# Kernel tuning notes

Measured on AMD Instinct MI355X. Metric: run time of the kernel, lower is better.

## Reference

```python
import jax, jax.numpy as jnp
import numpy as np

B, N = 1, 320  # embed_dim == seq_len == N is forced by the module's bmm shapes


def setup_inputs() -> dict:
    key = jax.random.key(0)
    k1, k2, k3, k4 = jax.random.split(key, 4)
    s = jax.random.normal(k1, (B, N, N), dtype=jnp.float32)
    futrue = jax.random.normal(k2, (B, N, N, N), dtype=jnp.float32)
    # nn.Linear(embed_dim, embed_dim) params
    lim = 1.0 / np.sqrt(N)
    W = jax.random.uniform(k3, (N, N), minval=-lim, maxval=lim, dtype=jnp.float32)
    b = jax.random.uniform(k4, (N,), minval=-lim, maxval=lim, dtype=jnp.float32)
    return {"s": s, "futrue": futrue, "W": W, "b": b}


def reference(s, futrue, W, b):
    # futrue = self.fc(futrue): Linear on last dim  [B,T,T,E]
    futP = jnp.einsum('bitj,ej->bite', futrue, W) + b
    # fc = s.transpose(1,2) @ futrue : [B,1,E,T] @ [B,T,T,E] -> [B,T,E,E]
    scores = jnp.einsum('bte,bitj->biej', s, futP)
    fc = jax.nn.softmax(scores, axis=-1)          # softmax over last dim
    # vectorized loop: t_i = fc[:, i].sum(1).unsqueeze(-2).bmm(s)
    w = fc.sum(axis=2)                            # [B, T, T] (sum over e)
    out = jnp.einsum('bij,bjk->bik', w, s)        # concat of all t_i -> [B, T, E]
    return out
```

## Files before the change

kernel.cpp:

```cpp
#include <hip/hip_runtime.h>
#include <hip/hip_bf16.h>
#include <math.h>

#define N 320
#define NN (N * N)
#define AST 328
#define SST 324

typedef float f32x16 __attribute__((ext_vector_type(16)));
typedef short s16x8  __attribute__((ext_vector_type(8)));

#define MFMA32(a, b, c) __builtin_amdgcn_mfma_f32_32x32x16_bf16((a), (b), (c), 0, 0, 0)

union U4V { uint4 q; s16x8 v; };
union UAV { unsigned u[4]; s16x8 v; };
union BFU { __hip_bfloat16 b; unsigned short u; };

__device__ inline void bsplit(float x, unsigned short& h, unsigned short& l) {
    __hip_bfloat16 hb = __float2bfloat16(x);
    float r = __bfloat162float(hb);
    __hip_bfloat16 lb = __float2bfloat16(x - r);
    BFU a; a.b = hb; h = a.u;
    BFU c; c.b = lb; l = c.u;
}
__device__ inline void split2(float x0, float x1, unsigned& hi, unsigned& lo) {
    unsigned short h0, l0, h1, l1;
    bsplit(x0, h0, l0); bsplit(x1, h1, l1);
    hi = (unsigned)h0 | ((unsigned)h1 << 16);
    lo = (unsigned)l0 | ((unsigned)l1 << 16);
}

__global__ __launch_bounds__(256) void zero_w_kernel(float* __restrict__ w) {
    int idx = blockIdx.x * 256 + threadIdx.x;
    ((float4*)w)[idx] = make_float4(0.f, 0.f, 0.f, 0.f);
}

__global__ __launch_bounds__(64) void colsum_kernel(const float* __restrict__ s,
                                                    float* __restrict__ colsum) {
    int e = blockIdx.x * 64 + threadIdx.x;
    float acc = 0.f;
    for (int t = 0; t < N; ++t) acc += s[t * N + e];
    colsum[e] = acc;
}

__global__ __launch_bounds__(64) void pack_s_kernel(const float* __restrict__ s,
                                                    uint4* __restrict__ spH,
                                                    uint4* __restrict__ spL) {
    int blk = blockIdx.x;
    int l = threadIdx.x;
    int et = blk / 20, ts = blk % 20;
    int e = et * 32 + (l & 31);
    int t0 = ts * 16 + (l >> 5) * 8;
    unsigned hi[4], lo[4];
#pragma unroll
    for (int d = 0; d < 4; ++d) {
        float x0 = s[(t0 + 2 * d) * N + e];
        float x1 = s[(t0 + 2 * d + 1) * N + e];
        split2(x0, x1, hi[d], lo[d]);
    }
    spH[blk * 64 + l] = make_uint4(hi[0], hi[1], hi[2], hi[3]);
    spL[blk * 64 + l] = make_uint4(lo[0], lo[1], lo[2], lo[3]);
}

__global__ __launch_bounds__(64) void pack_w_kernel(const float* __restrict__ W,
                                                    uint4* __restrict__ wpH,
                                                    uint4* __restrict__ wpL) {
    int blk = blockIdx.x;
    int l = threadIdx.x;
    int jt = blk / 20, ks = blk % 20;
    int j = jt * 32 + (l & 31);
    int k0 = ks * 16 + (l >> 5) * 8;
    const float* wr = W + (size_t)j * N + k0;
    unsigned hi[4], lo[4];
#pragma unroll
    for (int d = 0; d < 4; ++d) split2(wr[2 * d], wr[2 * d + 1], hi[d], lo[d]);
    wpH[blk * 64 + l] = make_uint4(hi[0], hi[1], hi[2], hi[3]);
    wpL[blk * 64 + l] = make_uint4(lo[0], lo[1], lo[2], lo[3]);
}

__global__ __launch_bounds__(640, 5) void fused_kernel(
    const float* __restrict__ fut,
    const uint4* __restrict__ spH, const uint4* __restrict__ spL,
    const uint4* __restrict__ wpH, const uint4* __restrict__ wpL,
    const float* __restrict__ bvec, const float* __restrict__ colsum,
    float* __restrict__ w)
{
    const int i   = blockIdx.y;
    const int et  = blockIdx.x;
    const int tid = threadIdx.x;
    const int wid = tid >> 6;
    const int lane = tid & 63;
    const int l31 = lane & 31;
    const int hf  = lane >> 5;

    __shared__ union {
        struct { unsigned short H[32 * AST]; unsigned short L[32 * AST]; } a;
        float S[32 * SST];
    } sm;
    __shared__ float csh[32];
    __shared__ float Mfin[32];
    __shared__ float Ifin[32];

    if (tid < 32) csh[tid] = colsum[et * 32 + tid];

    f32x16 acc;
#pragma unroll
    for (int r = 0; r < 16; ++r) acc[r] = 0.f;

    const float* fbase = fut + (size_t)i * NN + (size_t)(hf * 8) * N + wid * 32 + l31;
    const uint4* aH = spH + (size_t)(et * 20) * 64 + lane;
    const uint4* aL = spL + (size_t)(et * 20) * 64 + lane;

    for (int ts = 0; ts < 20; ++ts) {
        const float* fp = fbase + (size_t)(ts * 16) * N;
        float f[8];
#pragma unroll
        for (int j = 0; j < 8; ++j) f[j] = fp[j * N];
        U4V ah; ah.q = aH[ts * 64];
        U4V al; al.q = aL[ts * 64];
        UAV bh, bl;
#pragma unroll
        for (int d = 0; d < 4; ++d) split2(f[2 * d], f[2 * d + 1], bh.u[d], bl.u[d]);
        acc = MFMA32(ah.v, bh.v, acc);
        acc = MFMA32(al.v, bh.v, acc);
        acc = MFMA32(ah.v, bl.v, acc);
    }

#pragma unroll
    for (int r = 0; r < 16; ++r) {
        int e = (r & 3) + ((r >> 2) << 3) + (hf << 2);
        unsigned short h, l;
        bsplit(acc[r], h, l);
        sm.a.H[e * AST + wid * 32 + l31] = h;
        sm.a.L[e * AST + wid * 32 + l31] = l;
    }
    __syncthreads();

    f32x16 acc2;
#pragma unroll
    for (int r = 0; r < 16; ++r) acc2[r] = 0.f;

    const uint4* bH = wpH + (size_t)(wid * 20) * 64 + lane;
    const uint4* bL = wpL + (size_t)(wid * 20) * 64 + lane;

    for (int ks = 0; ks < 20; ++ks) {
        int aoff = l31 * AST + ks * 16 + hf * 8;
        s16x8 gah = *(const s16x8*)&sm.a.H[aoff];
        s16x8 gal = *(const s16x8*)&sm.a.L[aoff];
        U4V wh; wh.q = bH[ks * 64];
        U4V wl; wl.q = bL[ks * 64];
        acc2 = MFMA32(gah, wh.v, acc2);
        acc2 = MFMA32(gal, wh.v, acc2);
        acc2 = MFMA32(gah, wl.v, acc2);
    }

    const int jcol = wid * 32 + l31;
    float bj = bvec[jcol];
    float v[16];
#pragma unroll
    for (int r = 0; r < 16; ++r) {
        int e = (r & 3) + ((r >> 2) << 3) + (hf << 2);
        v[r] = acc2[r] + csh[e] * bj;
    }

    __syncthreads();

#pragma unroll
    for (int r = 0; r < 16; ++r) {
        int e = (r & 3) + ((r >> 2) << 3) + (hf << 2);
        sm.S[e * SST + jcol] = v[r];
    }
    __syncthreads();

    const int hw = tid >> 5;
    const int li = tid & 31;
    if (hw < 16) {
#pragma unroll
        for (int rr = 0; rr < 2; ++rr) {
            int row = 2 * hw + rr;
            float x[10];
            float m = -3.4e38f;
#pragma unroll
            for (int q = 0; q < 10; ++q) {
                x[q] = sm.S[row * SST + li + 32 * q];
                m = fmaxf(m, x[q]);
            }
#pragma unroll
            for (int off = 16; off; off >>= 1) m = fmaxf(m, __shfl_xor(m, off, 64));
            float ssum = 0.f;
#pragma unroll
            for (int q = 0; q < 10; ++q) ssum += __expf(x[q] - m);
#pragma unroll
            for (int off = 16; off; off >>= 1) ssum += __shfl_xor(ssum, off, 64);
            if (li == 0) { Mfin[row] = m; Ifin[row] = 1.0f / ssum; }
        }
    }
    __syncthreads();

    float wcol = 0.f;
#pragma unroll
    for (int r = 0; r < 16; ++r) {
        int e = (r & 3) + ((r >> 2) << 3) + (hf << 2);
        wcol += __expf(v[r] - Mfin[e]) * Ifin[e];
    }
    wcol += __shfl_xor(wcol, 32, 64);
    if (hf == 0) atomicAdd(&w[(size_t)i * N + jcol], wcol);
}

__global__ __launch_bounds__(64) void out_gemm_kernel(
    const float* __restrict__ w, const float* __restrict__ s,
    float* __restrict__ out)
{
    const int k = blockIdx.x * 64 + threadIdx.x;
    const int i = blockIdx.y;
    const float* wr = w + (size_t)i * N;
    float acc = 0.f;
    for (int j = 0; j < N; ++j) acc += wr[j] * s[j * N + k];
    out[(size_t)i * N + k] = acc;
}

extern "C" void kernel_launch(void* const* d_in, const int* in_sizes, int n_in,
                              void* d_out, int out_size, void* d_ws, size_t ws_size,
                              hipStream_t stream)
{
    const float* s    = (const float*)d_in[0];
    const float* fut  = (const float*)d_in[1];
    const float* W    = (const float*)d_in[2];
    const float* bvec = (const float*)d_in[3];
    float* out = (float*)d_out;

    char* base = (char*)d_ws;
    float* wbuf   = (float*)base;
    float* colsum = (float*)(base + 409600);
    uint4* spH = (uint4*)(base + 410880);
    uint4* spL = (uint4*)(base + 615680);
    uint4* wpH = (uint4*)(base + 820480);
    uint4* wpL = (uint4*)(base + 1025280);

    zero_w_kernel<<<dim3(NN / 4 / 256), dim3(256), 0, stream>>>(wbuf);
    colsum_kernel<<<dim3(N / 64), dim3(64), 0, stream>>>(s, colsum);
    pack_s_kernel<<<dim3(200), dim3(64), 0, stream>>>(s, spH, spL);
    pack_w_kernel<<<dim3(200), dim3(64), 0, stream>>>(W, wpH, wpL);

    fused_kernel<<<dim3(10, N), dim3(640), 0, stream>>>(
        fut, spH, spL, wpH, wpL, bvec, colsum, wbuf);

    out_gemm_kernel<<<dim3(N / 64, N), dim3(64), 0, stream>>>(wbuf, s, out);
}
```

Before: 451.6 us.

## Swizzle LDS staging, remap block order, cheapen bf16 split, parallelize small kernels

The fused kernel's intermediate now goes through a chunked, XOR-swizzled LDS layout instead of a padded row layout, to cut bank conflicts on the second GEMM's operand reads. The grid becomes 1D and is remapped so groups of 8 consecutive i values share an et tile. The bf16 hi/lo split now uses bit truncation instead of round-to-nearest conversions, which is fewer instructions but changes the rounding of the hi part. Colsum is split across row chunks and combined with atomics, and out_gemm uses wider blocks with four partial accumulators.

```diff
diff --git a/kernel.cpp b/kernel.cpp
--- a/kernel.cpp
+++ b/kernel.cpp
@@ -4,8 +4,8 @@
 
 #define N 320
 #define NN (N * N)
-#define AST 328
 #define SST 324
+#define ZCNT (NN + N)
 
 typedef float f32x16 __attribute__((ext_vector_type(16)));
 typedef short s16x8  __attribute__((ext_vector_type(8)));
@@ -14,33 +14,33 @@
 
 union U4V { uint4 q; s16x8 v; };
 union UAV { unsigned u[4]; s16x8 v; };
-union BFU { __hip_bfloat16 b; unsigned short u; };
-
-__device__ inline void bsplit(float x, unsigned short& h, unsigned short& l) {
-    __hip_bfloat16 hb = __float2bfloat16(x);
-    float r = __bfloat162float(hb);
-    __hip_bfloat16 lb = __float2bfloat16(x - r);
-    BFU a; a.b = hb; h = a.u;
-    BFU c; c.b = lb; l = c.u;
-}
+
 __device__ inline void split2(float x0, float x1, unsigned& hi, unsigned& lo) {
-    unsigned short h0, l0, h1, l1;
-    bsplit(x0, h0, l0); bsplit(x1, h1, l1);
-    hi = (unsigned)h0 | ((unsigned)h1 << 16);
-    lo = (unsigned)l0 | ((unsigned)l1 << 16);
+    unsigned u0 = __float_as_uint(x0), u1 = __float_as_uint(x1);
+    hi = (u0 >> 16) | (u1 & 0xFFFF0000u);
+    float d0 = x0 - __uint_as_float(u0 & 0xFFFF0000u);
+    float d1 = x1 - __uint_as_float(u1 & 0xFFFF0000u);
+    lo = (__float_as_uint(d0) >> 16) | (__float_as_uint(d1) & 0xFFFF0000u);
 }
 
 __global__ __launch_bounds__(256) void zero_w_kernel(float* __restrict__ w) {
     int idx = blockIdx.x * 256 + threadIdx.x;
-    ((float4*)w)[idx] = make_float4(0.f, 0.f, 0.f, 0.f);
+    if (idx * 4 < ZCNT) ((float4*)w)[idx] = make_float4(0.f, 0.f, 0.f, 0.f);
 }
 
 __global__ __launch_bounds__(64) void colsum_kernel(const float* __restrict__ s,
                                                     float* __restrict__ colsum) {
     int e = blockIdx.x * 64 + threadIdx.x;
-    float acc = 0.f;
-    for (int t = 0; t < N; ++t) acc += s[t * N + e];
-    colsum[e] = acc;
+    int t0 = blockIdx.y * 40;
+    float a[8];
+#pragma unroll
+    for (int u = 0; u < 8; ++u) a[u] = 0.f;
+    for (int t = 0; t < 40; t += 8) {
+#pragma unroll
+        for (int u = 0; u < 8; ++u) a[u] += s[(size_t)(t0 + t + u) * N + e];
+    }
+    float sum = ((a[0] + a[1]) + (a[2] + a[3])) + ((a[4] + a[5]) + (a[6] + a[7]));
+    atomicAdd(&colsum[e], sum);
 }
 
 __global__ __launch_bounds__(64) void pack_s_kernel(const float* __restrict__ s,
@@ -53,11 +53,9 @@
     int t0 = ts * 16 + (l >> 5) * 8;
     unsigned hi[4], lo[4];
 #pragma unroll
-    for (int d = 0; d < 4; ++d) {
-        float x0 = s[(t0 + 2 * d) * N + e];
-        float x1 = s[(t0 + 2 * d + 1) * N + e];
-        split2(x0, x1, hi[d], lo[d]);
-    }
+    for (int d = 0; d < 4; ++d)
+        split2(s[(size_t)(t0 + 2 * d) * N + e], s[(size_t)(t0 + 2 * d + 1) * N + e],
+               hi[d], lo[d]);
     spH[blk * 64 + l] = make_uint4(hi[0], hi[1], hi[2], hi[3]);
     spL[blk * 64 + l] = make_uint4(lo[0], lo[1], lo[2], lo[3]);
 }
@@ -85,8 +83,9 @@
     const float* __restrict__ bvec, const float* __restrict__ colsum,
     float* __restrict__ w)
 {
-    const int i   = blockIdx.y;
-    const int et  = blockIdx.x;
+    const int bid = blockIdx.x;
+    const int i   = (bid / 80) * 8 + (bid & 7);
+    const int et  = (bid >> 3) % 10;
     const int tid = threadIdx.x;
     const int wid = tid >> 6;
     const int lane = tid & 63;
@@ -94,7 +93,7 @@
     const int hf  = lane >> 5;
 
     __shared__ union {
-        struct { unsigned short H[32 * AST]; unsigned short L[32 * AST]; } a;
+        unsigned short G[2][40 * 32 * 8];
         float S[32 * SST];
     } sm;
     __shared__ float csh[32];
@@ -126,13 +125,22 @@
         acc = MFMA32(ah.v, bl.v, acc);
     }
 
-#pragma unroll
-    for (int r = 0; r < 16; ++r) {
-        int e = (r & 3) + ((r >> 2) << 3) + (hf << 2);
-        unsigned short h, l;
-        bsplit(acc[r], h, l);
-        sm.a.H[e * AST + wid * 32 + l31] = h;
-        sm.a.L[e * AST + wid * 32 + l31] = l;
+    {
+        const int c  = wid * 4 + (l31 >> 3);
+        const int jj = l31 & 7;
+        const int sw = c & 7;
+        unsigned short* GH = sm.G[0];
+        unsigned short* GL = sm.G[1];
+#pragma unroll
+        for (int r = 0; r < 16; ++r) {
+            int e = (r & 3) + ((r >> 2) << 3) + (hf << 2);
+            float x = acc[r];
+            unsigned u = __float_as_uint(x);
+            float d = x - __uint_as_float(u & 0xFFFF0000u);
+            int off = (c * 32 + (e ^ sw)) * 8 + jj;
+            GH[off] = (unsigned short)(u >> 16);
+            GL[off] = (unsigned short)(__float_as_uint(d) >> 16);
+        }
     }
     __syncthreads();
 
@@ -142,11 +150,15 @@
 
     const uint4* bH = wpH + (size_t)(wid * 20) * 64 + lane;
     const uint4* bL = wpL + (size_t)(wid * 20) * 64 + lane;
-
+    const unsigned short* GH = sm.G[0];
+    const unsigned short* GL = sm.G[1];
+
+#pragma unroll 4
     for (int ks = 0; ks < 20; ++ks) {
-        int aoff = l31 * AST + ks * 16 + hf * 8;
-        s16x8 gah = *(const s16x8*)&sm.a.H[aoff];
-        s16x8 gal = *(const s16x8*)&sm.a.L[aoff];
+        int c0 = ks * 2 + hf;
+        int aoff = (c0 * 32 + (l31 ^ (c0 & 7))) * 8;
+        s16x8 gah = *(const s16x8*)&GH[aoff];
+        s16x8 gal = *(const s16x8*)&GL[aoff];
         U4V wh; wh.q = bH[ks * 64];
         U4V wl; wl.q = bL[ks * 64];
         acc2 = MFMA32(gah, wh.v, acc2);
@@ -207,16 +219,21 @@
     if (hf == 0) atomicAdd(&w[(size_t)i * N + jcol], wcol);
 }
 
-__global__ __launch_bounds__(64) void out_gemm_kernel(
+__global__ __launch_bounds__(320) void out_gemm_kernel(
     const float* __restrict__ w, const float* __restrict__ s,
     float* __restrict__ out)
 {
-    const int k = blockIdx.x * 64 + threadIdx.x;
-    const int i = blockIdx.y;
+    const int i = blockIdx.x;
+    const int k = threadIdx.x;
     const float* wr = w + (size_t)i * N;
-    float acc = 0.f;
-    for (int j = 0; j < N; ++j) acc += wr[j] * s[j * N + k];
-    out[(size_t)i * N + k] = acc;
+    float a0 = 0.f, a1 = 0.f, a2 = 0.f, a3 = 0.f;
+    for (int j = 0; j < N; j += 4) {
+        a0 += wr[j + 0] * s[(size_t)(j + 0) * N + k];
+        a1 += wr[j + 1] * s[(size_t)(j + 1) * N + k];
+        a2 += wr[j + 2] * s[(size_t)(j + 2) * N + k];
+        a3 += wr[j + 3] * s[(size_t)(j + 3) * N + k];
+    }
+    out[(size_t)i * N + k] = (a0 + a1) + (a2 + a3);
 }
 
 extern "C" void kernel_launch(void* const* d_in, const int* in_sizes, int n_in,
@@ -237,13 +254,13 @@
     uint4* wpH = (uint4*)(base + 820480);
     uint4* wpL = (uint4*)(base + 1025280);
 
-    zero_w_kernel<<<dim3(NN / 4 / 256), dim3(256), 0, stream>>>(wbuf);
-    colsum_kernel<<<dim3(N / 64), dim3(64), 0, stream>>>(s, colsum);
+    zero_w_kernel<<<dim3((ZCNT / 4 + 255) / 256), dim3(256), 0, stream>>>(wbuf);
+    colsum_kernel<<<dim3(5, 8), dim3(64), 0, stream>>>(s, colsum);
     pack_s_kernel<<<dim3(200), dim3(64), 0, stream>>>(s, spH, spL);
     pack_w_kernel<<<dim3(200), dim3(64), 0, stream>>>(W, wpH, wpL);
 
-    fused_kernel<<<dim3(10, N), dim3(640), 0, stream>>>(
+    fused_kernel<<<dim3(3200), dim3(640), 0, stream>>>(
         fut, spH, spL, wpH, wpL, bvec, colsum, wbuf);
 
-    out_gemm_kernel<<<dim3(N / 64, N), dim3(64), 0, stream>>>(wbuf, s, out);
-}
+    out_gemm_kernel<<<dim3(N), dim3(320), 0, stream>>>(wbuf, s, out);
+}
```

Result: faster. 384.3 us (-14.9%).
